# Kernel tuning notes

Hardware: AMD Instinct MI355X
Metric: run time of the kernel (lower is better)

## Reference

```python
import jax, jax.numpy as jnp
import numpy as np

B, S, D, H, DFF = 4, 2048, 1024, 8, 4096
DH = D // H  # 128
EPS = 1e-5


def layernorm(x, gamma, beta):
    mu = jnp.mean(x, axis=-1, keepdims=True)
    var = jnp.mean(jnp.square(x - mu), axis=-1, keepdims=True)
    return (x - mu) * jax.lax.rsqrt(var + EPS) * gamma + beta


def setup_inputs() -> dict:
    key = jax.random.key(0)
    ks = jax.random.split(key, 6)
    s = 0.02
    return {
        "src": jax.random.normal(ks[0], (B, S, D), jnp.float32),
        "w_qkv": jax.random.normal(ks[1], (D, 3 * D), jnp.float32) * s,
        "w_out": jax.random.normal(ks[2], (D, D), jnp.float32) * s,
        "w1": jax.random.normal(ks[3], (D, DFF), jnp.float32) * s,
        "b1": jnp.zeros((DFF,), jnp.float32),
        "w2": jax.random.normal(ks[4], (DFF, D), jnp.float32) * s,
        "b2": jnp.zeros((D,), jnp.float32),
        "g1": jnp.ones((D,), jnp.float32),
        "beta1": jnp.zeros((D,), jnp.float32),
        "g2": jnp.ones((D,), jnp.float32),
        "beta2": jnp.zeros((D,), jnp.float32),
    }


def reference(src, w_qkv, w_out, w1, b1, w2, b2, g1, beta1, g2, beta2):
    b, s, d = src.shape
    # --- RingAttention == exact causal MHA on a single device ---
    qkv = src @ w_qkv  # [b, s, 3d]
    q, k, v = jnp.split(qkv, 3, axis=-1)
    to_heads = lambda x: x.reshape(b, s, H, DH).transpose(0, 2, 1, 3)  # [b,h,s,dh]
    q, k, v = to_heads(q), to_heads(k), to_heads(v)
    scale = 1.0 / jnp.sqrt(jnp.asarray(DH, src.dtype))
    scores = jnp.einsum('bhqd,bhkd->bhqk', q, k) * scale  # [b,h,s,s]
    causal = jnp.tril(jnp.ones((s, s), bool))
    neg = jnp.asarray(jnp.finfo(src.dtype).min, src.dtype)
    scores = jnp.where(causal, scores, neg)
    attn = jax.nn.softmax(scores, axis=-1)
    o = jnp.einsum('bhqk,bhkd->bhqd', attn, v)  # [b,h,s,dh]
    o = o.transpose(0, 2, 1, 3).reshape(b, s, d) @ w_out
    # dropout layers are identity at inference
    x = layernorm(src + o, g1, beta1)
    ff = jax.nn.relu(x @ w1 + b1) @ w2 + b2
    return layernorm(x + ff, g2, beta2)
```

## Files before the change

kernel.cpp:

```cpp
#include <hip/hip_runtime.h>

typedef unsigned short u16;
typedef __attribute__((ext_vector_type(8))) short short8;
typedef __attribute__((ext_vector_type(4))) float float4v;

#define MFMA_BF16(a, b, c) __builtin_amdgcn_mfma_f32_16x16x32_bf16((a), (b), (c), 0, 0, 0)

#define B_ 4
#define S_ 2048
#define D_ 1024
#define H_ 8
#define DH_ 128
#define DFF_ 4096
#define EPS_ 1e-5f
#define ROWS_ (B_ * S_)
#define CSCALE_ 0.12751672939502f

__device__ __forceinline__ u16 f2bf(float f) {
  union { float f; unsigned u; } x; x.f = f;
  unsigned r = x.u + 0x7fffu + ((x.u >> 16) & 1u);
  return (u16)(r >> 16);
}

typedef __attribute__((address_space(1))) const unsigned int guint;
typedef __attribute__((address_space(3))) unsigned int luint;
__device__ __forceinline__ void gl2lds16(const u16* g, u16* l) {
  __builtin_amdgcn_global_load_lds((guint*)g, (luint*)l, 16, 0, 0);
}

__global__ void cast_bf16_kernel(const float* __restrict__ in, u16* __restrict__ out, int n4) {
  int i = blockIdx.x * blockDim.x + threadIdx.x;
  int stride = gridDim.x * blockDim.x;
  for (; i < n4; i += stride) {
    float4 v = ((const float4*)in)[i];
    ushort4 u;
    u.x = f2bf(v.x); u.y = f2bf(v.y); u.z = f2bf(v.z); u.w = f2bf(v.w);
    ((ushort4*)out)[i] = u;
  }
}

__global__ void transpose_cast_kernel(const float* __restrict__ in, u16* __restrict__ out,
                                      int K, int N) {
  __shared__ float t[32][33];
  int k0 = blockIdx.x * 32, n0 = blockIdx.y * 32;
  int tx = threadIdx.x & 31, ty = threadIdx.x >> 5;
  #pragma unroll
  for (int i = 0; i < 4; ++i)
    t[ty + 8 * i][tx] = in[(size_t)(k0 + ty + 8 * i) * N + n0 + tx];
  __syncthreads();
  #pragma unroll
  for (int i = 0; i < 4; ++i)
    out[(size_t)(n0 + ty + 8 * i) * K + k0 + tx] = f2bf(t[tx][ty + 8 * i]);
}

__global__ void transpose_v_kernel(const u16* __restrict__ in, u16* __restrict__ out) {
  __shared__ u16 t[32][33];
  int s0 = blockIdx.x * 32, d0 = blockIdx.y * 32, bh = blockIdx.z;
  const u16* src = in + (size_t)bh * S_ * DH_;
  u16* dst = out + (size_t)bh * DH_ * S_;
  int tx = threadIdx.x & 31, ty = threadIdx.x >> 5;
  #pragma unroll
  for (int i = 0; i < 4; ++i)
    t[ty + 8 * i][tx] = src[(size_t)(s0 + ty + 8 * i) * DH_ + d0 + tx];
  __syncthreads();
  #pragma unroll
  for (int i = 0; i < 4; ++i)
    dst[(size_t)(d0 + ty + 8 * i) * S_ + s0 + tx] = t[tx][ty + 8 * i];
}

template <int MODE>
__global__ __launch_bounds__(512, 2) void gemm256_kernel(
    const u16* __restrict__ A, const u16* __restrict__ Bt,
    const int M, const int N, const int K,
    float* __restrict__ outF, u16* __restrict__ outH, const float* __restrict__ bias,
    u16* __restrict__ qo, u16* __restrict__ ko, u16* __restrict__ vo) {
  extern __shared__ u16 smem[];
  u16* At  = smem;
  u16* Bts = smem + 2 * 256 * 64;
  const int tid = threadIdx.x;
  const int lane = tid & 63, wave = tid >> 6;
  const int quad = lane >> 4, r16 = lane & 15;
  const int halfw = wave >> 2;
  const int wn = (wave & 3) * 64;
  const int m0 = blockIdx.x * 256, n0 = blockIdx.y * 256;
  const int NT = K >> 6;

  const int rowin = wave * 8 + (lane >> 3);
  const int sc = lane & 7;
  const int shalf = rowin >> 5, srr = rowin & 31;

  const u16* Asrc[4];
  const u16* Bsrc[4];
  #pragma unroll
  for (int u = 0; u < 4; ++u) {
    const int ra = shalf * 128 + u * 32 + srr;
    Asrc[u] = A + (size_t)(m0 + ra) * K + (sc ^ (ra & 7)) * 8;
    const int rb = u * 64 + rowin;
    Bsrc[u] = Bt + (size_t)(n0 + rb) * K + (sc ^ (rb & 7)) * 8;
  }

  float4v acc[8][4];
  #pragma unroll
  for (int i = 0; i < 8; ++i)
    #pragma unroll
    for (int j = 0; j < 4; ++j) acc[i][j] = (float4v)0.0f;

#define STAGE_A(t, u) gl2lds16(Asrc[u] + (t) * 64, At  + ((t) & 1) * 16384 + (u) * 4096 + wave * 512)
#define STAGE_B(t, u) gl2lds16(Bsrc[u] + (t) * 64, Bts + ((t) & 1) * 16384 + (u) * 4096 + wave * 512)

  STAGE_B(0, 0); STAGE_B(0, 1); STAGE_B(0, 2); STAGE_B(0, 3);
  STAGE_A(0, 0); STAGE_A(0, 1); STAGE_A(0, 2); STAGE_A(0, 3);
  if (NT > 1) {
    STAGE_B(1, 0); STAGE_B(1, 1); STAGE_B(1, 2); STAGE_B(1, 3);
    STAGE_A(1, 0); STAGE_A(1, 1);
    asm volatile("s_waitcnt vmcnt(6)" ::: "memory");
  } else {
    asm volatile("s_waitcnt vmcnt(0)" ::: "memory");
  }
  __builtin_amdgcn_s_barrier();

  for (int kt = 0; kt < NT; ++kt) {
    const u16* Ab = At + (kt & 1) * 16384;
    const u16* Bb = Bts + (kt & 1) * 16384;
    short8 bfr[4][2];
    #pragma unroll
    for (int q = 0; q < 4; ++q) {
      if (q == 0) {
        #pragma unroll
        for (int j = 0; j < 4; ++j)
          #pragma unroll
          for (int s = 0; s < 2; ++s)
            bfr[j][s] = *(const short8*)(Bb + (wn + j * 16 + r16) * 64 +
                                         (((s * 4 + quad) ^ (r16 & 7)) * 8));
      }
      short8 af[2][2];
      #pragma unroll
      for (int di = 0; di < 2; ++di)
        #pragma unroll
        for (int s = 0; s < 2; ++s)
          af[di][s] = *(const short8*)(Ab + (q * 64 + halfw * 32 + di * 16 + r16) * 64 +
                                       (((s * 4 + quad) ^ (r16 & 7)) * 8));
      if (q == 0)      { if (kt + 1 < NT) { STAGE_A(kt + 1, 2); STAGE_A(kt + 1, 3); } }
      else if (q == 1) { if (kt + 2 < NT) { STAGE_B(kt + 2, 0); STAGE_B(kt + 2, 1); } }
      else if (q == 2) { if (kt + 2 < NT) { STAGE_B(kt + 2, 2); STAGE_B(kt + 2, 3); } }
      else             { if (kt + 2 < NT) { STAGE_A(kt + 2, 0); STAGE_A(kt + 2, 1); } }
      __builtin_amdgcn_s_barrier();
      asm volatile("s_waitcnt lgkmcnt(0)" ::: "memory");
      __builtin_amdgcn_s_setprio(1);
      #pragma unroll
      for (int j = 0; j < 4; ++j) {
        acc[2 * q][j]     = MFMA_BF16(af[0][0], bfr[j][0], acc[2 * q][j]);
        acc[2 * q][j]     = MFMA_BF16(af[0][1], bfr[j][1], acc[2 * q][j]);
        acc[2 * q + 1][j] = MFMA_BF16(af[1][0], bfr[j][0], acc[2 * q + 1][j]);
        acc[2 * q + 1][j] = MFMA_BF16(af[1][1], bfr[j][1], acc[2 * q + 1][j]);
      }
      __builtin_amdgcn_s_setprio(0);
      if (q == 3) {
        if (kt + 2 < NT)      { asm volatile("s_waitcnt vmcnt(6)" ::: "memory"); }
        else if (kt + 1 < NT) { asm volatile("s_waitcnt vmcnt(0)" ::: "memory"); }
      }
      __builtin_amdgcn_s_barrier();
    }
  }
#undef STAGE_A
#undef STAGE_B

  #pragma unroll
  for (int i = 0; i < 8; ++i) {
    const int rowb = m0 + halfw * 128 + i * 16 + quad * 4;
    #pragma unroll
    for (int j = 0; j < 4; ++j) {
      const int col = n0 + wn + j * 16 + r16;
      #pragma unroll
      for (int rg = 0; rg < 4; ++rg) {
        float val = acc[i][j][rg];
        const int r = rowb + rg;
        if (MODE == 0) {
          const int part = col >> 10, cc = col & 1023;
          const int h = cc >> 7, dh = cc & 127;
          const int b = r >> 11, s = r & 2047;
          u16* dst = (part == 0) ? qo : (part == 1) ? ko : vo;
          if (part == 0) val *= CSCALE_;
          dst[((size_t)(b * H_ + h) * S_ + s) * DH_ + dh] = f2bf(val);
        } else if (MODE == 1) {
          outF[(size_t)r * N + col] = val;
        } else if (MODE == 2) {
          val += bias[col];
          val = fmaxf(val, 0.0f);
          outH[(size_t)r * N + col] = f2bf(val);
        } else {
          val += bias[col];
          outF[(size_t)r * N + col] = val;
        }
      }
    }
  }
}

__global__ __launch_bounds__(256) void attn_kernel(
    const u16* __restrict__ Q, const u16* __restrict__ Kg,
    const u16* __restrict__ Vtg, u16* __restrict__ O) {
  __shared__ u16 Ks[64][136];
  __shared__ u16 Vt[128][72];
  __shared__ u16 Pw[4][16][72];
  const int tid = threadIdx.x;
  const int lane = tid & 63, wave = tid >> 6;
  const int quad = lane >> 4, r16 = lane & 15;
  const int pairIdx = blockIdx.x;
  const int bh = blockIdx.y;
  const size_t base = (size_t)bh * S_ * DH_;
  const size_t vtb = (size_t)bh * DH_ * S_;
  const int b = bh >> 3, h = bh & 7;

  const u16* kg0 = Kg + base + (size_t)(tid >> 4) * DH_ + (tid & 15) * 8;
  u16* ksl = &Ks[tid >> 4][(tid & 15) * 8];
  const u16* vg0 = Vtg + vtb + (size_t)(tid >> 3) * S_ + (tid & 7) * 8;
  u16* vtl = &Vt[tid >> 3][(tid & 7) * 8];

  for (int half = 0; half < 2; ++half) {
    const int qb = (half == 0) ? pairIdx : 31 - pairIdx;
    const int qr = qb * 64 + wave * 16 + r16;

    short8 aq[4];
    #pragma unroll
    for (int ks = 0; ks < 4; ++ks)
      aq[ks] = *(const short8*)(Q + base + (size_t)qr * DH_ + ks * 32 + quad * 8);

    float4v acco[8];
    #pragma unroll
    for (int i = 0; i < 8; ++i) acco[i] = (float4v)0.0f;
    float m_q = -1e30f, l_q = 0.0f;

    for (int kb = 0; kb <= qb; ++kb) {
      __syncthreads();
      #pragma unroll
      for (int i = 0; i < 4; ++i)
        *(short8*)(ksl + i * 16 * 136) =
            *(const short8*)(kg0 + (size_t)(kb * 64 + i * 16) * DH_);
      #pragma unroll
      for (int i = 0; i < 4; ++i)
        *(short8*)(vtl + i * 32 * 72) =
            *(const short8*)(vg0 + (size_t)i * 32 * S_ + kb * 64);
      __syncthreads();

      float4v accs[4];
      #pragma unroll
      for (int t = 0; t < 4; ++t) accs[t] = (float4v)0.0f;
      #pragma unroll
      for (int ks = 0; ks < 4; ++ks) {
        #pragma unroll
        for (int t = 0; t < 4; ++t) {
          short8 ak = *(const short8*)&Ks[t * 16 + r16][ks * 32 + quad * 8];
          accs[t] = MFMA_BF16(ak, aq[ks], accs[t]);
        }
      }
      if (kb == qb) {
        #pragma unroll
        for (int t = 0; t < 4; ++t)
          #pragma unroll
          for (int rg = 0; rg < 4; ++rg) {
            int kc = kb * 64 + t * 16 + quad * 4 + rg;
            if (kc > qr) accs[t][rg] = -1e30f;
          }
      }
      float mv = accs[0][0];
      #pragma unroll
      for (int t = 0; t < 4; ++t)
        #pragma unroll
        for (int rg = 0; rg < 4; ++rg) mv = fmaxf(mv, accs[t][rg]);
      mv = fmaxf(mv, __shfl_xor(mv, 16));
      mv = fmaxf(mv, __shfl_xor(mv, 32));
      const float mnew = fmaxf(m_q, mv);
      const float alpha = __builtin_amdgcn_exp2f(m_q - mnew);
      float s0 = 0.0f;
      #pragma unroll
      for (int t = 0; t < 4; ++t)
        #pragma unroll
        for (int rg = 0; rg < 4; ++rg) {
          float p = __builtin_amdgcn_exp2f(accs[t][rg] - mnew);
          accs[t][rg] = p;
          s0 += p;
        }
      s0 += __shfl_xor(s0, 16);
      s0 += __shfl_xor(s0, 32);
      l_q = l_q * alpha + s0;
      m_q = mnew;

      #pragma unroll
      for (int t = 0; t < 4; ++t) {
        union { float f; unsigned u; } c0, c1, c2, c3;
        c0.f = accs[t][0]; c1.f = accs[t][1]; c2.f = accs[t][2]; c3.f = accs[t][3];
        uint2 pk;
        pk.x = ((c0.u + 0x8000u) >> 16) | ((c1.u + 0x8000u) & 0xffff0000u);
        pk.y = ((c2.u + 0x8000u) >> 16) | ((c3.u + 0x8000u) & 0xffff0000u);
        *(uint2*)&Pw[wave][r16][t * 16 + quad * 4] = pk;
      }
      float al[4];
      #pragma unroll
      for (int rg = 0; rg < 4; ++rg) al[rg] = __shfl(alpha, quad * 4 + rg);
      #pragma unroll
      for (int nt = 0; nt < 8; ++nt)
        #pragma unroll
        for (int rg = 0; rg < 4; ++rg) acco[nt][rg] *= al[rg];
      asm volatile("s_waitcnt lgkmcnt(0)" ::: "memory");
      #pragma unroll
      for (int ks2 = 0; ks2 < 2; ++ks2) {
        short8 ap = *(const short8*)&Pw[wave][r16][ks2 * 32 + quad * 8];
        #pragma unroll
        for (int nt = 0; nt < 8; ++nt) {
          short8 bv = *(const short8*)&Vt[nt * 16 + r16][ks2 * 32 + quad * 8];
          acco[nt] = MFMA_BF16(ap, bv, acco[nt]);
        }
      }
    }

    float lr[4];
    #pragma unroll
    for (int rg = 0; rg < 4; ++rg) lr[rg] = __shfl(l_q, quad * 4 + rg);
    const int sbase = qb * 64 + wave * 16 + quad * 4;
    #pragma unroll
    for (int nt = 0; nt < 8; ++nt)
      #pragma unroll
      for (int rg = 0; rg < 4; ++rg) {
        float val = acco[nt][rg] / lr[rg];
        O[((size_t)(b * S_ + sbase + rg)) * D_ + h * DH_ + nt * 16 + r16] = f2bf(val);
      }
  }
}

__global__ __launch_bounds__(256) void ln_kernel(
    const float* __restrict__ a, const float* __restrict__ res,
    const float* __restrict__ g, const float* __restrict__ be,
    float* __restrict__ xf, u16* __restrict__ xb) {
  __shared__ float red[8];
  const int row = blockIdx.x, tid = threadIdx.x;
  const float4 va = ((const float4*)(a + (size_t)row * D_))[tid];
  const float4 vr = ((const float4*)(res + (size_t)row * D_))[tid];
  float4 v;
  v.x = va.x + vr.x; v.y = va.y + vr.y; v.z = va.z + vr.z; v.w = va.w + vr.w;
  float s = v.x + v.y + v.z + v.w;
  float q = v.x * v.x + v.y * v.y + v.z * v.z + v.w * v.w;
  #pragma unroll
  for (int m = 1; m < 64; m <<= 1) {
    s += __shfl_xor(s, m);
    q += __shfl_xor(q, m);
  }
  const int wave = tid >> 6, lane = tid & 63;
  if (lane == 0) { red[wave] = s; red[4 + wave] = q; }
  __syncthreads();
  s = red[0] + red[1] + red[2] + red[3];
  q = red[4] + red[5] + red[6] + red[7];
  const float mu = s * (1.0f / D_);
  const float var = q * (1.0f / D_) - mu * mu;
  const float inv = rsqrtf(var + EPS_);
  const float4 gg = ((const float4*)g)[tid];
  const float4 bb = ((const float4*)be)[tid];
  float4 y;
  y.x = (v.x - mu) * inv * gg.x + bb.x;
  y.y = (v.y - mu) * inv * gg.y + bb.y;
  y.z = (v.z - mu) * inv * gg.z + bb.z;
  y.w = (v.w - mu) * inv * gg.w + bb.w;
  ((float4*)(xf + (size_t)row * D_))[tid] = y;
  if (xb) {
    ushort4 u;
    u.x = f2bf(y.x); u.y = f2bf(y.y); u.z = f2bf(y.z); u.w = f2bf(y.w);
    ((ushort4*)(xb + (size_t)row * D_))[tid] = u;
  }
}

extern "C" void kernel_launch(void* const* d_in, const int* in_sizes, int n_in,
                              void* d_out, int out_size, void* d_ws, size_t ws_size,
                              hipStream_t stream) {
  const float* src   = (const float*)d_in[0];
  const float* w_qkv = (const float*)d_in[1];
  const float* w_out = (const float*)d_in[2];
  const float* w1    = (const float*)d_in[3];
  const float* b1    = (const float*)d_in[4];
  const float* w2    = (const float*)d_in[5];
  const float* b2    = (const float*)d_in[6];
  const float* g1    = (const float*)d_in[7];
  const float* be1   = (const float*)d_in[8];
  const float* g2    = (const float*)d_in[9];
  const float* be2   = (const float*)d_in[10];
  float* out = (float*)d_out;

  char* ws = (char*)d_ws;
  size_t off = 0;
  auto alloc = [&](size_t bytes) -> void* {
    void* p = ws + off;
    off += (bytes + 255) & ~(size_t)255;
    return p;
  };
  u16* src_bf = (u16*)alloc((size_t)ROWS_ * D_ * 2);
  u16* wqkvT  = (u16*)alloc((size_t)3 * D_ * D_ * 2);
  u16* woutT  = (u16*)alloc((size_t)D_ * D_ * 2);
  u16* w1T    = (u16*)alloc((size_t)DFF_ * D_ * 2);
  u16* w2T    = (u16*)alloc((size_t)D_ * DFF_ * 2);
  u16* qbuf   = (u16*)alloc((size_t)ROWS_ * D_ * 2);
  u16* kbuf   = (u16*)alloc((size_t)ROWS_ * D_ * 2);
  u16* vbuf   = (u16*)alloc((size_t)ROWS_ * D_ * 2);
  u16* obuf   = (u16*)alloc((size_t)ROWS_ * D_ * 2);
  u16* vT     = (u16*)alloc((size_t)ROWS_ * D_ * 2);
  float* proj = (float*)alloc((size_t)ROWS_ * D_ * 4);
  float* xf   = (float*)alloc((size_t)ROWS_ * D_ * 4);
  u16* xb     = (u16*)alloc((size_t)ROWS_ * D_ * 2);
  u16* h1     = qbuf;
  float* ff   = proj;

  const int GSMEM = 131072;
  hipFuncSetAttribute((const void*)gemm256_kernel<0>, hipFuncAttributeMaxDynamicSharedMemorySize, GSMEM);
  hipFuncSetAttribute((const void*)gemm256_kernel<1>, hipFuncAttributeMaxDynamicSharedMemorySize, GSMEM);
  hipFuncSetAttribute((const void*)gemm256_kernel<2>, hipFuncAttributeMaxDynamicSharedMemorySize, GSMEM);
  hipFuncSetAttribute((const void*)gemm256_kernel<3>, hipFuncAttributeMaxDynamicSharedMemorySize, GSMEM);

  cast_bf16_kernel<<<2048, 256, 0, stream>>>(src, src_bf, ROWS_ * D_ / 4);
  transpose_cast_kernel<<<dim3(D_ / 32, 3 * D_ / 32), 256, 0, stream>>>(w_qkv, wqkvT, D_, 3 * D_);
  transpose_cast_kernel<<<dim3(D_ / 32, D_ / 32), 256, 0, stream>>>(w_out, woutT, D_, D_);
  transpose_cast_kernel<<<dim3(D_ / 32, DFF_ / 32), 256, 0, stream>>>(w1, w1T, D_, DFF_);
  transpose_cast_kernel<<<dim3(DFF_ / 32, D_ / 32), 256, 0, stream>>>(w2, w2T, DFF_, D_);

  gemm256_kernel<0><<<dim3(ROWS_ / 256, 3 * D_ / 256), 512, GSMEM, stream>>>(
      src_bf, wqkvT, ROWS_, 3 * D_, D_, nullptr, nullptr, nullptr, qbuf, kbuf, vbuf);
  transpose_v_kernel<<<dim3(S_ / 32, DH_ / 32, B_ * H_), 256, 0, stream>>>(vbuf, vT);
  attn_kernel<<<dim3(16, B_ * H_), 256, 0, stream>>>(qbuf, kbuf, vT, obuf);
  gemm256_kernel<1><<<dim3(ROWS_ / 256, D_ / 256), 512, GSMEM, stream>>>(
      obuf, woutT, ROWS_, D_, D_, proj, nullptr, nullptr, nullptr, nullptr, nullptr);
  ln_kernel<<<ROWS_, 256, 0, stream>>>(proj, src, g1, be1, xf, xb);
  gemm256_kernel<2><<<dim3(ROWS_ / 256, DFF_ / 256), 512, GSMEM, stream>>>(
      xb, w1T, ROWS_, DFF_, D_, nullptr, h1, b1, nullptr, nullptr, nullptr);
  gemm256_kernel<3><<<dim3(ROWS_ / 256, D_ / 256), 512, GSMEM, stream>>>(
      h1, w2T, ROWS_, D_, DFF_, ff, nullptr, b2, nullptr, nullptr, nullptr);
  ln_kernel<<<ROWS_, 256, 0, stream>>>(ff, xf, g2, be2, out, nullptr);
}
```

Baseline: 544.6 us.

## Add 256x128-tile GEMM variant for QKV, out-proj and FFN2 GEMMs

Adds a second GEMM kernel using 256x128 output tiles with 96KB LDS, launch bounds allowing two blocks per CU, and a split A-stage pipeline. The QKV, output-projection and second FFN GEMMs switch to it, doubling block counts for the N=1024 GEMMs, which previously launched only 128 blocks on a 256-CU device. This improves CU occupancy and wave-level parallelism at the cost of less B-operand reuse per tile and more global traffic.

```diff
diff --git a/kernel.cpp b/kernel.cpp
--- a/kernel.cpp
+++ b/kernel.cpp
@@ -175,6 +175,143 @@
       for (int rg = 0; rg < 4; ++rg) {
         float val = acc[i][j][rg];
         const int r = rowb + rg;
+        if (MODE == 2) {
+          val += bias[col];
+          val = fmaxf(val, 0.0f);
+          outH[(size_t)r * N + col] = f2bf(val);
+        } else {
+          outF[(size_t)r * N + col] = val;
+        }
+      }
+    }
+  }
+}
+
+template <int MODE>
+__global__ __launch_bounds__(512, 2) void gemm256x128_kernel(
+    const u16* __restrict__ A, const u16* __restrict__ Bt,
+    const int M, const int N, const int K,
+    float* __restrict__ outF, u16* __restrict__ outH, const float* __restrict__ bias,
+    u16* __restrict__ qo, u16* __restrict__ ko, u16* __restrict__ vo) {
+  extern __shared__ u16 smem[];
+  u16* At  = smem;
+  u16* Bts = smem + 2 * 256 * 64;
+  const int tid = threadIdx.x;
+  const int lane = tid & 63, wave = tid >> 6;
+  const int quad = lane >> 4, r16 = lane & 15;
+  const int w64 = wave >> 1;
+  const int wn = (wave & 1) * 64;
+  const int m0 = blockIdx.x * 256, n0 = blockIdx.y * 128;
+  const int NT = K >> 6;
+
+  const int rowin = wave * 8 + (lane >> 3);
+  const int sc = lane & 7;
+
+  const u16* Asrc[4];
+  const u16* Bsrc[2];
+  #pragma unroll
+  for (int u = 0; u < 4; ++u) {
+    const int ra = ((u & 1) * 2 + (rowin >> 5)) * 64 + (u >> 1) * 32 + (rowin & 31);
+    Asrc[u] = A + (size_t)(m0 + ra) * K + (sc ^ (ra & 7)) * 8;
+  }
+  #pragma unroll
+  for (int u = 0; u < 2; ++u) {
+    const int rb = u * 64 + rowin;
+    Bsrc[u] = Bt + (size_t)(n0 + rb) * K + (sc ^ (rb & 7)) * 8;
+  }
+
+  float4v acc[4][4];
+  #pragma unroll
+  for (int i = 0; i < 4; ++i)
+    #pragma unroll
+    for (int j = 0; j < 4; ++j) acc[i][j] = (float4v)0.0f;
+
+#define STAGE_A(t, u) gl2lds16(Asrc[u] + (t) * 64, At  + ((t) & 1) * 16384 + (u) * 4096 + wave * 512)
+#define STAGE_B(t, u) gl2lds16(Bsrc[u] + (t) * 64, Bts + ((t) & 1) * 8192 + (u) * 4096 + wave * 512)
+
+  STAGE_B(0, 0); STAGE_B(0, 1); STAGE_A(0, 0); STAGE_A(0, 1);
+  STAGE_A(0, 2); STAGE_A(0, 3);
+  STAGE_B(1, 0); STAGE_B(1, 1); STAGE_A(1, 0); STAGE_A(1, 1);
+  asm volatile("s_waitcnt vmcnt(6)" ::: "memory");
+  __builtin_amdgcn_s_barrier();
+
+  for (int kt = 0; kt < NT; ++kt) {
+    const u16* Ab = At + (kt & 1) * 16384;
+    const u16* Bb = Bts + (kt & 1) * 8192;
+    short8 bfr[4][2];
+    #pragma unroll
+    for (int j = 0; j < 4; ++j)
+      #pragma unroll
+      for (int s = 0; s < 2; ++s)
+        bfr[j][s] = *(const short8*)(Bb + (wn + j * 16 + r16) * 64 +
+                                     (((s * 4 + quad) ^ (r16 & 7)) * 8));
+    {
+      short8 af[2][2];
+      #pragma unroll
+      for (int di = 0; di < 2; ++di)
+        #pragma unroll
+        for (int s = 0; s < 2; ++s)
+          af[di][s] = *(const short8*)(Ab + (w64 * 32 + di * 16 + r16) * 64 +
+                                       (((s * 4 + quad) ^ (r16 & 7)) * 8));
+      if (kt + 1 < NT) { STAGE_A(kt + 1, 2); STAGE_A(kt + 1, 3); }
+      __builtin_amdgcn_s_barrier();
+      asm volatile("s_waitcnt lgkmcnt(0)" ::: "memory");
+      __builtin_amdgcn_s_setprio(1);
+      #pragma unroll
+      for (int j = 0; j < 4; ++j) {
+        acc[0][j] = MFMA_BF16(af[0][0], bfr[j][0], acc[0][j]);
+        acc[0][j] = MFMA_BF16(af[0][1], bfr[j][1], acc[0][j]);
+        acc[1][j] = MFMA_BF16(af[1][0], bfr[j][0], acc[1][j]);
+        acc[1][j] = MFMA_BF16(af[1][1], bfr[j][1], acc[1][j]);
+      }
+      __builtin_amdgcn_s_setprio(0);
+      if (kt + 1 < NT) { asm volatile("s_waitcnt vmcnt(6)" ::: "memory"); }
+      else             { asm volatile("s_waitcnt vmcnt(0)" ::: "memory"); }
+      __builtin_amdgcn_s_barrier();
+    }
+    {
+      short8 af[2][2];
+      #pragma unroll
+      for (int di = 0; di < 2; ++di)
+        #pragma unroll
+        for (int s = 0; s < 2; ++s)
+          af[di][s] = *(const short8*)(Ab + (128 + w64 * 32 + di * 16 + r16) * 64 +
+                                       (((s * 4 + quad) ^ (r16 & 7)) * 8));
+      if (kt + 2 < NT) {
+        STAGE_B(kt + 2, 0); STAGE_B(kt + 2, 1);
+        STAGE_A(kt + 2, 0); STAGE_A(kt + 2, 1);
+      }
+      __builtin_amdgcn_s_barrier();
+      asm volatile("s_waitcnt lgkmcnt(0)" ::: "memory");
+      __builtin_amdgcn_s_setprio(1);
+      #pragma unroll
+      for (int j = 0; j < 4; ++j) {
+        acc[2][j] = MFMA_BF16(af[0][0], bfr[j][0], acc[2][j]);
+        acc[2][j] = MFMA_BF16(af[0][1], bfr[j][1], acc[2][j]);
+        acc[3][j] = MFMA_BF16(af[1][0], bfr[j][0], acc[3][j]);
+        acc[3][j] = MFMA_BF16(af[1][1], bfr[j][1], acc[3][j]);
+      }
+      __builtin_amdgcn_s_setprio(0);
+      if (kt + 1 < NT) {
+        if (kt + 2 < NT) { asm volatile("s_waitcnt vmcnt(6)" ::: "memory"); }
+        else             { asm volatile("s_waitcnt vmcnt(2)" ::: "memory"); }
+      }
+      __builtin_amdgcn_s_barrier();
+    }
+  }
+#undef STAGE_A
+#undef STAGE_B
+
+  #pragma unroll
+  for (int i = 0; i < 4; ++i) {
+    const int rowb = m0 + w64 * 64 + i * 16 + quad * 4;
+    #pragma unroll
+    for (int j = 0; j < 4; ++j) {
+      const int col = n0 + wn + j * 16 + r16;
+      #pragma unroll
+      for (int rg = 0; rg < 4; ++rg) {
+        float val = acc[i][j][rg];
+        const int r = rowb + rg;
         if (MODE == 0) {
           const int part = col >> 10, cc = col & 1023;
           const int h = cc >> 7, dh = cc & 127;
@@ -184,10 +321,6 @@
           dst[((size_t)(b * H_ + h) * S_ + s) * DH_ + dh] = f2bf(val);
         } else if (MODE == 1) {
           outF[(size_t)r * N + col] = val;
-        } else if (MODE == 2) {
-          val += bias[col];
-          val = fmaxf(val, 0.0f);
-          outH[(size_t)r * N + col] = f2bf(val);
         } else {
           val += bias[col];
           outF[(size_t)r * N + col] = val;
@@ -407,11 +540,12 @@
   u16* h1     = qbuf;
   float* ff   = proj;
 
-  const int GSMEM = 131072;
-  hipFuncSetAttribute((const void*)gemm256_kernel<0>, hipFuncAttributeMaxDynamicSharedMemorySize, GSMEM);
-  hipFuncSetAttribute((const void*)gemm256_kernel<1>, hipFuncAttributeMaxDynamicSharedMemorySize, GSMEM);
+  const int GSMEM  = 131072;
+  const int GSMEM2 = 98304;
   hipFuncSetAttribute((const void*)gemm256_kernel<2>, hipFuncAttributeMaxDynamicSharedMemorySize, GSMEM);
-  hipFuncSetAttribute((const void*)gemm256_kernel<3>, hipFuncAttributeMaxDynamicSharedMemorySize, GSMEM);
+  hipFuncSetAttribute((const void*)gemm256x128_kernel<0>, hipFuncAttributeMaxDynamicSharedMemorySize, GSMEM2);
+  hipFuncSetAttribute((const void*)gemm256x128_kernel<1>, hipFuncAttributeMaxDynamicSharedMemorySize, GSMEM2);
+  hipFuncSetAttribute((const void*)gemm256x128_kernel<3>, hipFuncAttributeMaxDynamicSharedMemorySize, GSMEM2);
 
   cast_bf16_kernel<<<2048, 256, 0, stream>>>(src, src_bf, ROWS_ * D_ / 4);
   transpose_cast_kernel<<<dim3(D_ / 32, 3 * D_ / 32), 256, 0, stream>>>(w_qkv, wqkvT, D_, 3 * D_);
@@ -419,16 +553,16 @@
   transpose_cast_kernel<<<dim3(D_ / 32, DFF_ / 32), 256, 0, stream>>>(w1, w1T, D_, DFF_);
   transpose_cast_kernel<<<dim3(DFF_ / 32, D_ / 32), 256, 0, stream>>>(w2, w2T, DFF_, D_);
 
-  gemm256_kernel<0><<<dim3(ROWS_ / 256, 3 * D_ / 256), 512, GSMEM, stream>>>(
+  gemm256x128_kernel<0><<<dim3(ROWS_ / 256, 3 * D_ / 128), 512, GSMEM2, stream>>>(
       src_bf, wqkvT, ROWS_, 3 * D_, D_, nullptr, nullptr, nullptr, qbuf, kbuf, vbuf);
   transpose_v_kernel<<<dim3(S_ / 32, DH_ / 32, B_ * H_), 256, 0, stream>>>(vbuf, vT);
   attn_kernel<<<dim3(16, B_ * H_), 256, 0, stream>>>(qbuf, kbuf, vT, obuf);
-  gemm256_kernel<1><<<dim3(ROWS_ / 256, D_ / 256), 512, GSMEM, stream>>>(
+  gemm256x128_kernel<1><<<dim3(ROWS_ / 256, D_ / 128), 512, GSMEM2, stream>>>(
       obuf, woutT, ROWS_, D_, D_, proj, nullptr, nullptr, nullptr, nullptr, nullptr);
   ln_kernel<<<ROWS_, 256, 0, stream>>>(proj, src, g1, be1, xf, xb);
   gemm256_kernel<2><<<dim3(ROWS_ / 256, DFF_ / 256), 512, GSMEM, stream>>>(
       xb, w1T, ROWS_, DFF_, D_, nullptr, h1, b1, nullptr, nullptr, nullptr);
-  gemm256_kernel<3><<<dim3(ROWS_ / 256, D_ / 256), 512, GSMEM, stream>>>(
+  gemm256x128_kernel<3><<<dim3(ROWS_ / 256, D_ / 128), 512, GSMEM2, stream>>>(
       h1, w2T, ROWS_, D_, DFF_, ff, nullptr, b2, nullptr, nullptr, nullptr);
   ln_kernel<<<ROWS_, 256, 0, stream>>>(ff, xf, g2, be2, out, nullptr);
 }
```

Measured after the change: 499.1 us. 8.4% less time.
